# Performance work log

Hardware: AMD Instinct MI355X
Metric: run time of the kernel (lower is better)

Reference implementation:

```python
import jax, jax.numpy as jnp
import numpy as np

N_NODES = 50000
N_EDGES = 400000
D_NODE = 256
D_EDGE = 64
LN_EPS = 1e-6  # flax LayerNorm default


def _layer_norm(x, scale, bias):
    mu = jnp.mean(x, axis=-1, keepdims=True)
    var = jnp.mean(jnp.square(x - mu), axis=-1, keepdims=True)
    return (x - mu) * jax.lax.rsqrt(var + LN_EPS) * scale + bias


def _glorot(key, shape):
    fan_in, fan_out = shape
    std = jnp.sqrt(2.0 / (fan_in + fan_out))
    return std * jax.random.normal(key, shape, dtype=jnp.float32)


def setup_inputs() -> dict:
    key = jax.random.key(0)
    ks = jax.random.split(key, 10)
    inp = {
        "nodes": jax.random.normal(ks[0], (N_NODES, D_NODE), dtype=jnp.float32),
        "edges": jax.random.normal(ks[1], (N_EDGES, D_EDGE), dtype=jnp.float32),
        "senders": jax.random.randint(ks[2], (N_EDGES,), 0, N_NODES, dtype=jnp.int32),
        "receivers": jax.random.randint(ks[3], (N_EDGES,), 0, N_NODES, dtype=jnp.int32),
        # message projection (no bias)
        "W_message": _glorot(ks[4], (D_NODE + D_EDGE, D_NODE)),
        # NodeMLP (ReluMLP_skip) with n_features_list_nodes = [256, 256, 256]
        "mlp_W0": _glorot(ks[5], (D_NODE, D_NODE)), "mlp_b0": jnp.zeros((D_NODE,), jnp.float32),
        "mlp_W1": _glorot(ks[6], (D_NODE, D_NODE)), "mlp_b1": jnp.zeros((D_NODE,), jnp.float32),
        "mlp_W2": _glorot(ks[7], (D_NODE, D_NODE)), "mlp_b2": jnp.zeros((D_NODE,), jnp.float32),
        # LayerNorm params
        "ln_aggr_scale": jnp.ones((D_NODE,), jnp.float32), "ln_aggr_bias": jnp.zeros((D_NODE,), jnp.float32),
        "ln_out_scale": jnp.ones((D_NODE,), jnp.float32), "ln_out_bias": jnp.zeros((D_NODE,), jnp.float32),
    }
    return inp


def _relu_mlp_skip(x, Ws, bs):
    # Dense layers; ReLU on all but the last; residual add whenever widths match.
    n = len(Ws)
    for i, (W, b) in enumerate(zip(Ws, bs)):
        y = x @ W + b
        if i < n - 1:
            y = jax.nn.relu(y)
        x = x + y if y.shape[-1] == x.shape[-1] else y
    return x


def reference(nodes, edges, senders, receivers, W_message,
              mlp_W0, mlp_b0, mlp_W1, mlp_b1, mlp_W2, mlp_b2,
              ln_aggr_scale, ln_aggr_bias, ln_out_scale, ln_out_bias):
    total_nodes = nodes.shape[0]
    sender_features = nodes[senders]                      # [E, d] gather
    msg_in = jnp.concatenate([sender_features, edges], axis=-1)  # [E, d+d_e]
    messages = msg_in @ W_message                          # [E, d]
    agg = jax.ops.segment_sum(messages, receivers, num_segments=total_nodes)  # [N, d]
    h = _layer_norm(jax.nn.relu(agg) + nodes, ln_aggr_scale, ln_aggr_bias)
    nodes_out = _relu_mlp_skip(h, [mlp_W0, mlp_W1, mlp_W2], [mlp_b0, mlp_b1, mlp_b2])
    nodes_new = _layer_norm(nodes + nodes_out, ln_out_scale, ln_out_bias)
    return nodes_new
```

## Files before the change

### kernel.cpp

```cpp
#include <hip/hip_runtime.h>

#define NN 50000
#define NE 400000

typedef unsigned short u16;
typedef unsigned int   u32;
typedef __bf16 bf16x4 __attribute__((ext_vector_type(4)));
typedef __bf16 bf16x8 __attribute__((ext_vector_type(8)));
typedef float  f32x4  __attribute__((ext_vector_type(4)));

union ABFrag { bf16x8 v; bf16x4 h[2]; };
union BFrag  { uint4 u; bf16x8 v; };

__device__ __forceinline__ u16 f2bfu(float f) {
  u32 u = __builtin_bit_cast(u32, f);
  return (u16)((u + 0x7FFFu + ((u >> 16) & 1u)) >> 16);
}
__device__ __forceinline__ float bf2f(u16 u) {
  return __builtin_bit_cast(float, (u32)u << 16);
}

__device__ __forceinline__ void pack_one(const float* __restrict__ W,
                                         u16* __restrict__ P, int idx) {
  int k = idx >> 8, n = idx & 255;
  int t = k >> 5, kp = k & 31;
  int g = (kp & 15) >> 2;
  int j = (kp & 3) | ((kp >> 4) << 2);
  P[(((t << 8) + n) << 5) + (g << 3) + j] = f2bfu(W[idx]);
}

#define NB_CVT  12500
#define NB_PACK 1088
#define NB_HIST 1563

__global__ __launch_bounds__(256) void k_prep(
    const float* __restrict__ nodes, u16* __restrict__ nodes_bf,
    const float* __restrict__ Wm, const float* __restrict__ W0,
    const float* __restrict__ W1, const float* __restrict__ W2,
    u16* __restrict__ Pm, u16* __restrict__ P0,
    u16* __restrict__ P1, u16* __restrict__ P2,
    const int* __restrict__ recv, int* __restrict__ cnt)
{
  int b = blockIdx.x, t = threadIdx.x;
  if (b < NB_CVT) {
    int i = b * 256 + t;
    float4 f = ((const float4*)nodes)[i];
    ushort4 o;
    o.x = f2bfu(f.x); o.y = f2bfu(f.y); o.z = f2bfu(f.z); o.w = f2bfu(f.w);
    ((ushort4*)nodes_bf)[i] = o;
  } else if (b < NB_CVT + NB_PACK) {
    int idx = (b - NB_CVT) * 256 + t;
    const int S0 = 320 * 256, S1 = S0 + 65536, S2 = S1 + 65536;
    if (idx < S0)      pack_one(Wm, Pm, idx);
    else if (idx < S1) pack_one(W0, P0, idx - S0);
    else if (idx < S2) pack_one(W1, P1, idx - S1);
    else               pack_one(W2, P2, idx - S2);
  } else {
    int i = (b - NB_CVT - NB_PACK) * 256 + t;
    if (i < NE) atomicAdd(&cnt[recv[i]], 1);
  }
}

__global__ __launch_bounds__(256) void k_scan1(const int* __restrict__ cnt,
                                               int* __restrict__ loc,
                                               int* __restrict__ bsum) {
  __shared__ int sm[256];
  int t = threadIdx.x, i = blockIdx.x * 256 + t;
  int v = (i < NN) ? cnt[i] : 0;
  sm[t] = v;
  __syncthreads();
  #pragma unroll
  for (int d = 1; d < 256; d <<= 1) {
    int x = sm[t];
    int y = (t >= d) ? sm[t - d] : 0;
    __syncthreads();
    sm[t] = x + y;
    __syncthreads();
  }
  if (i < NN) loc[i] = sm[t] - v;
  if (t == 255) bsum[blockIdx.x] = sm[255];
}

__global__ __launch_bounds__(256) void k_scan2(int* __restrict__ bsum,
                                               int* __restrict__ bpre, int nb) {
  __shared__ int sm[256];
  int t = threadIdx.x;
  int v = (t < nb) ? bsum[t] : 0;
  sm[t] = v;
  __syncthreads();
  #pragma unroll
  for (int d = 1; d < 256; d <<= 1) {
    int x = sm[t];
    int y = (t >= d) ? sm[t - d] : 0;
    __syncthreads();
    sm[t] = x + y;
    __syncthreads();
  }
  if (t < nb) bpre[t] = sm[t] - v;
}

__global__ __launch_bounds__(256) void k_scan3(const int* __restrict__ loc,
                                               const int* __restrict__ bpre,
                                               int* __restrict__ offs,
                                               int* __restrict__ cursor) {
  int i = blockIdx.x * 256 + threadIdx.x;
  if (i < NN) {
    int o = loc[i] + bpre[blockIdx.x];
    offs[i] = o;
    cursor[i] = o;
  }
  if (i == NN - 1) offs[NN] = NE;
}

__global__ __launch_bounds__(256) void k_scatter(
    const int* __restrict__ snd, const int* __restrict__ recv,
    int* __restrict__ cursor, int* __restrict__ s_snd, int* __restrict__ s_eid) {
  int e = blockIdx.x * 256 + threadIdx.x;
  if (e < NE) {
    int p = atomicAdd(&cursor[recv[e]], 1);
    s_snd[p] = snd[e];
    s_eid[p] = e;
  }
}


#define AT_ADDR(r, c) (atb + ((((r) * 640) + ((c) * 2)) ^ (((r) & 7) << 4)))

#define WRBT(c, v) do { int _c = (c); \
  int _i = (((_c >> 10) << 13) + ((_c & 3) << 11) + (((_c & 1023) >> 2) << 3)) ^ ((_c & 3) << 4); \
  *(uint4*)&Bt[_i] = (v); } while (0)

#define MFMA_STEP(t) \
  _Pragma("unroll") \
  for (int kk = 0; kk < 2; ++kk) { \
    ABFrag a; \
    const int kc = (((t) * 2 + kk) << 5) + (g << 2); \
    const int m = wr16 + l16; \
    a.h[0] = *(const bf16x4*)AT_ADDR(m, kc); \
    a.h[1] = *(const bf16x4*)AT_ADDR(m, kc + 16); \
    _Pragma("unroll") \
    for (int q = 0; q < 4; ++q) { \
      BFrag b; \
      b.u = *(const uint4*)&Bt[((kk << 13) + (g << 11) + ((wcn + (q << 4) + l16) << 3)) ^ (g << 4)]; \
      acc[q] = __builtin_amdgcn_mfma_f32_16x16x32_bf16(a.v, b.v, acc[q], 0, 0, 0); \
    } \
  }

#define RUN_LAYER(wp, T) do { \
  const u16* pb = (wp) + ((size_t)tid << 3); \
  uint4 p0 = *(const uint4*)(pb); \
  uint4 p1 = *(const uint4*)(pb + 8192); \
  _Pragma("unroll 1") \
  for (int t = 0; t < (T); ++t) { \
    __syncthreads(); \
    WRBT(tid, p0); WRBT(tid + 1024, p1); \
    if (t + 1 < (T)) { \
      const u16* nb = pb + ((size_t)(t + 1) << 14); \
      p0 = *(const uint4*)nb; p1 = *(const uint4*)(nb + 8192); \
    } \
    __syncthreads(); \
    MFMA_STEP(t) \
  } \
} while (0)

#define LN_STATS() do { \
  _Pragma("unroll") \
  for (int r = 0; r < 4; ++r) { \
    float s  = acc[0][r] + acc[1][r] + acc[2][r] + acc[3][r]; \
    float s2 = acc[0][r]*acc[0][r] + acc[1][r]*acc[1][r] + acc[2][r]*acc[2][r] + acc[3][r]*acc[3][r]; \
    s  += __shfl_xor(s, 1);  s  += __shfl_xor(s, 2);  s  += __shfl_xor(s, 4);  s  += __shfl_xor(s, 8); \
    s2 += __shfl_xor(s2, 1); s2 += __shfl_xor(s2, 2); s2 += __shfl_xor(s2, 4); s2 += __shfl_xor(s2, 8); \
    if (l16 == 0) { int m = wr16 + g4 + r; red[m][wc2] = s; red[m][wc2 + 1] = s2; } \
  } \
  __syncthreads(); \
  if (tid < 64) { \
    float s  = red[tid][0] + red[tid][2] + red[tid][4] + red[tid][6]; \
    float s2 = red[tid][1] + red[tid][3] + red[tid][5] + red[tid][7]; \
    float mu  = s * (1.f / 256.f); \
    float var = s2 * (1.f / 256.f) - mu * mu; \
    murs[tid][0] = mu; murs[tid][1] = rsqrtf(var + 1e-6f); \
  } \
  __syncthreads(); \
} while (0)

__global__ __launch_bounds__(1024)
void k_fused(
    const u16* __restrict__ nodes_bf, const float* __restrict__ edges,
    const int* __restrict__ offs, const int* __restrict__ s_snd,
    const int* __restrict__ s_eid,
    const float* __restrict__ nodes,
    const u16* __restrict__ wm, const u16* __restrict__ w0,
    const u16* __restrict__ w1, const u16* __restrict__ w2,
    const float* __restrict__ b0, const float* __restrict__ b1,
    const float* __restrict__ b2,
    const float* __restrict__ lnAs, const float* __restrict__ lnAb,
    const float* __restrict__ lnOs, const float* __restrict__ lnOb,
    float* __restrict__ out)
{
  __shared__ u16 At[64 * 320];
  __shared__ u16 Bt[16384];
  __shared__ float red[64][8];
  __shared__ float murs[64][2];

  const int tid = threadIdx.x;
  const int lane = tid & 63;
  const int w16 = tid >> 6;
  const int wr16 = (w16 >> 2) << 4;
  const int wcn = (w16 & 3) << 6;
  const int wc2 = (w16 & 3) << 1;
  const int l16 = lane & 15, g = lane >> 4, g4 = g << 2;
  const int r0 = blockIdx.x * 64;

  char* const atb = (char*)At;

  {
    const int m0 = w16 << 2;
    #pragma unroll 1
    for (int i = 0; i < 4; ++i) {
      const int m = m0 + i;
      const int node = r0 + m;
      float a0 = 0.f, a1 = 0.f, a2 = 0.f, a3 = 0.f, a4 = 0.f;
      if (node < NN) {
        int beg = offs[node], end = offs[node + 1];
        int j = beg;
        for (; j + 1 < end; j += 2) {
          int sA = s_snd[j],     eA = s_eid[j];
          int sB = s_snd[j + 1], eB = s_eid[j + 1];
          ushort4 nA = *(const ushort4*)(nodes_bf + (size_t)sA * 256 + (lane << 2));
          ushort4 nB = *(const ushort4*)(nodes_bf + (size_t)sB * 256 + (lane << 2));
          float evA = edges[(size_t)eA * 64 + lane];
          float evB = edges[(size_t)eB * 64 + lane];
          a0 += bf2f(nA.x) + bf2f(nB.x); a1 += bf2f(nA.y) + bf2f(nB.y);
          a2 += bf2f(nA.z) + bf2f(nB.z); a3 += bf2f(nA.w) + bf2f(nB.w);
          a4 += evA + evB;
        }
        if (j < end) {
          int sA = s_snd[j], eA = s_eid[j];
          ushort4 nA = *(const ushort4*)(nodes_bf + (size_t)sA * 256 + (lane << 2));
          a0 += bf2f(nA.x); a1 += bf2f(nA.y); a2 += bf2f(nA.z); a3 += bf2f(nA.w);
          a4 += edges[(size_t)eA * 64 + lane];
        }
      }
      ushort4 o;
      o.x = f2bfu(a0); o.y = f2bfu(a1); o.z = f2bfu(a2); o.w = f2bfu(a3);
      *(ushort4*)AT_ADDR(m, lane << 2) = o;
      *(u16*)AT_ADDR(m, 256 + lane) = f2bfu(a4);
    }
  }

  f32x4 acc[4];
  const f32x4 z = {0.f, 0.f, 0.f, 0.f};
  #pragma unroll
  for (int q = 0; q < 4; ++q) acc[q] = z;

  RUN_LAYER(wm, 5);

  #pragma unroll
  for (int q = 0; q < 4; ++q) {
    int n = wcn + (q << 4) + l16;
    #pragma unroll
    for (int r = 0; r < 4; ++r) {
      int row = r0 + wr16 + g4 + r;
      float nv = (row < NN) ? nodes[(size_t)row * 256 + n] : 0.f;
      acc[q][r] = fmaxf(acc[q][r], 0.f) + nv;
    }
  }
  LN_STATS();
  #pragma unroll
  for (int q = 0; q < 4; ++q) {
    int n = wcn + (q << 4) + l16;
    float scl = lnAs[n], bia = lnAb[n];
    #pragma unroll
    for (int r = 0; r < 4; ++r) {
      int m = wr16 + g4 + r;
      float h = (acc[q][r] - murs[m][0]) * murs[m][1] * scl + bia;
      *(u16*)AT_ADDR(m, n) = f2bfu(h);
      acc[q][r] = 0.f;
    }
  }

  #pragma unroll 1
  for (int l = 0; l < 3; ++l) {
    const u16* wp = (l == 0) ? w0 : (l == 1) ? w1 : w2;
    RUN_LAYER(wp, 4);
    __syncthreads();

    if (l < 2) {
      const float* bp = (l == 0) ? b0 : b1;
      #pragma unroll
      for (int q = 0; q < 4; ++q) {
        int n = wcn + (q << 4) + l16;
        float bn = bp[n];
        #pragma unroll
        for (int r = 0; r < 4; ++r) {
          int m = wr16 + g4 + r;
          u16* p = (u16*)AT_ADDR(m, n);
          float xn = bf2f(*p) + fmaxf(acc[q][r] + bn, 0.f);
          *p = f2bfu(xn);
          acc[q][r] = 0.f;
        }
      }
    } else {
      #pragma unroll
      for (int q = 0; q < 4; ++q) {
        int n = wcn + (q << 4) + l16;
        float bn = b2[n];
        #pragma unroll
        for (int r = 0; r < 4; ++r) {
          int m = wr16 + g4 + r;
          int row = r0 + m;
          float nv = (row < NN) ? nodes[(size_t)row * 256 + n] : 0.f;
          acc[q][r] = nv + bf2f(*(const u16*)AT_ADDR(m, n)) + acc[q][r] + bn;
        }
      }
    }
  }

  LN_STATS();
  #pragma unroll
  for (int q = 0; q < 4; ++q) {
    int n = wcn + (q << 4) + l16;
    float scl = lnOs[n], bia = lnOb[n];
    #pragma unroll
    for (int r = 0; r < 4; ++r) {
      int m = wr16 + g4 + r;
      int row = r0 + m;
      if (row < NN)
        out[(size_t)row * 256 + n] =
            (acc[q][r] - murs[m][0]) * murs[m][1] * scl + bia;
    }
  }
}

extern "C" void kernel_launch(void* const* d_in, const int* in_sizes, int n_in,
                              void* d_out, int out_size, void* d_ws, size_t ws_size,
                              hipStream_t stream)
{
  const float* nodes = (const float*)d_in[0];
  const float* edges = (const float*)d_in[1];
  const int* senders = (const int*)d_in[2];
  const int* receivers = (const int*)d_in[3];
  const float* Wmsg = (const float*)d_in[4];
  const float* W0 = (const float*)d_in[5];
  const float* b0 = (const float*)d_in[6];
  const float* W1 = (const float*)d_in[7];
  const float* b1 = (const float*)d_in[8];
  const float* W2 = (const float*)d_in[9];
  const float* b2 = (const float*)d_in[10];
  const float* lnAs = (const float*)d_in[11];
  const float* lnAb = (const float*)d_in[12];
  const float* lnOs = (const float*)d_in[13];
  const float* lnOb = (const float*)d_in[14];
  float* out = (float*)d_out;
  (void)in_sizes; (void)n_in; (void)out_size; (void)ws_size;

  char* w = (char*)d_ws;
  size_t off = 0;
  auto take = [&](size_t b) { void* p = w + off; off += (b + 511) & ~(size_t)511; return p; };

  u16*   nodes_bf = (u16*)take((size_t)NN * 256 * 2);
  u16*   wmsg_p   = (u16*)take(320 * 256 * 2);
  u16*   w0_p     = (u16*)take(256 * 256 * 2);
  u16*   w1_p     = (u16*)take(256 * 256 * 2);
  u16*   w2_p     = (u16*)take(256 * 256 * 2);
  int*   cnt      = (int*)take((size_t)NN * 4);
  int*   loc      = (int*)take((size_t)NN * 4);
  int*   offs     = (int*)take((size_t)(NN + 1) * 4);
  int*   cursor   = (int*)take((size_t)NN * 4);
  int*   s_snd    = (int*)take((size_t)NE * 4);
  int*   s_eid    = (int*)take((size_t)NE * 4);
  int*   bsum     = (int*)take(256 * 4);
  int*   bpre     = (int*)take(256 * 4);

  const int NB = (NN + 255) / 256;

  hipMemsetAsync(cnt, 0, (size_t)NN * 4, stream);
  k_prep<<<NB_CVT + NB_PACK + NB_HIST, 256, 0, stream>>>(
      nodes, nodes_bf, Wmsg, W0, W1, W2, wmsg_p, w0_p, w1_p, w2_p,
      receivers, cnt);

  k_scan1<<<NB, 256, 0, stream>>>(cnt, loc, bsum);
  k_scan2<<<1, 256, 0, stream>>>(bsum, bpre, NB);
  k_scan3<<<NB, 256, 0, stream>>>(loc, bpre, offs, cursor);
  k_scatter<<<(NE + 255) / 256, 256, 0, stream>>>(senders, receivers, cursor, s_snd, s_eid);

  const int MB = (NN + 63) / 64;
  k_fused<<<MB, 1024, 0, stream>>>(nodes_bf, edges, offs, s_snd, s_eid,
                                   nodes, wmsg_p, w0_p, w1_p, w2_p,
                                   b0, b1, b2, lnAs, lnAb, lnOs, lnOb, out);
}
```

Before: 235.2 us.

## Split gather-aggregation into separate prefetching kernel before fused MLP kernel

Moves the per-node gather/sum of sender features and edge features out of the fused GEMM kernel into a new k_aggr kernel. It processes 4 consecutive nodes per wavefront with a software-pipelined, 4-deep prefetch of edge loads and writes a bf16 [N,320] buffer. The fused kernel then just loads that buffer into LDS, so its 1024-thread blocks no longer stall on irregular gathers. The weight prefetch in the layer loop is moved after the second barrier. This costs an extra ~32MB write+read round trip through global memory and one more kernel launch.

```diff
diff --git a/kernel.cpp b/kernel.cpp
--- a/kernel.cpp
+++ b/kernel.cpp
@@ -123,6 +123,60 @@
   }
 }
 
+__global__ __launch_bounds__(256) void k_aggr(
+    const u16* __restrict__ nodes_bf, const float* __restrict__ edges,
+    const int* __restrict__ offs, const int* __restrict__ s_snd,
+    const int* __restrict__ s_eid, u16* __restrict__ X)
+{
+  const int wid = blockIdx.x * 4 + (threadIdx.x >> 6);
+  const int lane = threadIdx.x & 63;
+  const int n0 = wid * 4;
+  const int o0 = offs[n0], b1 = offs[n0 + 1], b2 = offs[n0 + 2],
+            b3 = offs[n0 + 3], o4 = offs[n0 + 4];
+
+  float a0 = 0.f, a1 = 0.f, a2 = 0.f, a3 = 0.f, a4 = 0.f;
+  int cur = 0;
+
+#define AGLD(J, NV, EV) do { int _j = (J); if (_j < o4) { \
+    int _s = s_snd[_j], _e = s_eid[_j]; \
+    NV = *(const ushort4*)(nodes_bf + (size_t)_s * 256 + (lane << 2)); \
+    EV = edges[(size_t)_e * 64 + lane]; } } while (0)
+
+#define AGFLUSH(NODE) do { \
+    ushort4 _o; _o.x = f2bfu(a0); _o.y = f2bfu(a1); _o.z = f2bfu(a2); _o.w = f2bfu(a3); \
+    u16* _xr = X + (size_t)(NODE) * 320; \
+    *(ushort4*)(_xr + (lane << 2)) = _o; \
+    _xr[256 + lane] = f2bfu(a4); \
+    a0 = 0.f; a1 = 0.f; a2 = 0.f; a3 = 0.f; a4 = 0.f; } while (0)
+
+#define AGCONS(J, NV, EV) do { int _j = (J); if (_j < o4) { \
+    if (cur == 0 && _j == b1) { AGFLUSH(n0);     cur = 1; } \
+    if (cur == 1 && _j == b2) { AGFLUSH(n0 + 1); cur = 2; } \
+    if (cur == 2 && _j == b3) { AGFLUSH(n0 + 2); cur = 3; } \
+    a0 += bf2f(NV.x); a1 += bf2f(NV.y); a2 += bf2f(NV.z); a3 += bf2f(NV.w); \
+    a4 += EV; } } while (0)
+
+  ushort4 v0 = {0,0,0,0}, v1 = {0,0,0,0}, v2 = {0,0,0,0}, v3 = {0,0,0,0};
+  float e0 = 0.f, e1 = 0.f, e2 = 0.f, e3 = 0.f;
+  AGLD(o0 + 0, v0, e0); AGLD(o0 + 1, v1, e1);
+  AGLD(o0 + 2, v2, e2); AGLD(o0 + 3, v3, e3);
+
+  for (int jb = o0; jb < o4; jb += 4) {
+    ushort4 w0 = {0,0,0,0}, w1 = {0,0,0,0}, w2 = {0,0,0,0}, w3 = {0,0,0,0};
+    float f0 = 0.f, f1 = 0.f, f2 = 0.f, f3 = 0.f;
+    AGLD(jb + 4, w0, f0); AGLD(jb + 5, w1, f1);
+    AGLD(jb + 6, w2, f2); AGLD(jb + 7, w3, f3);
+    AGCONS(jb + 0, v0, e0); AGCONS(jb + 1, v1, e1);
+    AGCONS(jb + 2, v2, e2); AGCONS(jb + 3, v3, e3);
+    v0 = w0; v1 = w1; v2 = w2; v3 = w3;
+    e0 = f0; e1 = f1; e2 = f2; e3 = f3;
+  }
+  for (int k = cur; k < 4; ++k) AGFLUSH(n0 + k);
+#undef AGLD
+#undef AGFLUSH
+#undef AGCONS
+}
+
 
 #define AT_ADDR(r, c) (atb + ((((r) * 640) + ((c) * 2)) ^ (((r) & 7) << 4)))
 
@@ -154,11 +208,11 @@
   for (int t = 0; t < (T); ++t) { \
     __syncthreads(); \
     WRBT(tid, p0); WRBT(tid + 1024, p1); \
-    if (t + 1 < (T)) { \
+    __syncthreads(); \
+    if (t + 1 < (T)) {                      \
       const u16* nb = pb + ((size_t)(t + 1) << 14); \
       p0 = *(const uint4*)nb; p1 = *(const uint4*)(nb + 8192); \
     } \
-    __syncthreads(); \
     MFMA_STEP(t) \
   } \
 } while (0)
@@ -185,10 +239,7 @@
 
 __global__ __launch_bounds__(1024)
 void k_fused(
-    const u16* __restrict__ nodes_bf, const float* __restrict__ edges,
-    const int* __restrict__ offs, const int* __restrict__ s_snd,
-    const int* __restrict__ s_eid,
-    const float* __restrict__ nodes,
+    const u16* __restrict__ X, const float* __restrict__ nodes,
     const u16* __restrict__ wm, const u16* __restrict__ w0,
     const u16* __restrict__ w1, const u16* __restrict__ w2,
     const float* __restrict__ b0, const float* __restrict__ b1,
@@ -213,38 +264,15 @@
 
   char* const atb = (char*)At;
 
-  {
-    const int m0 = w16 << 2;
-    #pragma unroll 1
-    for (int i = 0; i < 4; ++i) {
-      const int m = m0 + i;
-      const int node = r0 + m;
-      float a0 = 0.f, a1 = 0.f, a2 = 0.f, a3 = 0.f, a4 = 0.f;
-      if (node < NN) {
-        int beg = offs[node], end = offs[node + 1];
-        int j = beg;
-        for (; j + 1 < end; j += 2) {
-          int sA = s_snd[j],     eA = s_eid[j];
-          int sB = s_snd[j + 1], eB = s_eid[j + 1];
-          ushort4 nA = *(const ushort4*)(nodes_bf + (size_t)sA * 256 + (lane << 2));
-          ushort4 nB = *(const ushort4*)(nodes_bf + (size_t)sB * 256 + (lane << 2));
-          float evA = edges[(size_t)eA * 64 + lane];
-          float evB = edges[(size_t)eB * 64 + lane];
-          a0 += bf2f(nA.x) + bf2f(nB.x); a1 += bf2f(nA.y) + bf2f(nB.y);
-          a2 += bf2f(nA.z) + bf2f(nB.z); a3 += bf2f(nA.w) + bf2f(nB.w);
-          a4 += evA + evB;
-        }
-        if (j < end) {
-          int sA = s_snd[j], eA = s_eid[j];
-          ushort4 nA = *(const ushort4*)(nodes_bf + (size_t)sA * 256 + (lane << 2));
-          a0 += bf2f(nA.x); a1 += bf2f(nA.y); a2 += bf2f(nA.z); a3 += bf2f(nA.w);
-          a4 += edges[(size_t)eA * 64 + lane];
-        }
-      }
-      ushort4 o;
-      o.x = f2bfu(a0); o.y = f2bfu(a1); o.z = f2bfu(a2); o.w = f2bfu(a3);
-      *(ushort4*)AT_ADDR(m, lane << 2) = o;
-      *(u16*)AT_ADDR(m, 256 + lane) = f2bfu(a4);
+  #pragma unroll
+  for (int it = 0; it < 3; ++it) {
+    int c = tid + it * 1024;
+    if (c < 2560) {
+      int r = c / 40, seg = c - r * 40;
+      int row = r0 + r;
+      uint4 v = {0u, 0u, 0u, 0u};
+      if (row < NN) v = *(const uint4*)(X + (size_t)row * 320 + seg * 8);
+      *(uint4*)(atb + ((r * 640 + seg * 16) ^ ((r & 7) << 4))) = v;
     }
   }
 
@@ -363,6 +391,7 @@
   u16*   w0_p     = (u16*)take(256 * 256 * 2);
   u16*   w1_p     = (u16*)take(256 * 256 * 2);
   u16*   w2_p     = (u16*)take(256 * 256 * 2);
+  u16*   X        = (u16*)take((size_t)NN * 320 * 2);
   int*   cnt      = (int*)take((size_t)NN * 4);
   int*   loc      = (int*)take((size_t)NN * 4);
   int*   offs     = (int*)take((size_t)(NN + 1) * 4);
@@ -384,8 +413,9 @@
   k_scan3<<<NB, 256, 0, stream>>>(loc, bpre, offs, cursor);
   k_scatter<<<(NE + 255) / 256, 256, 0, stream>>>(senders, receivers, cursor, s_snd, s_eid);
 
+  k_aggr<<<NN / 16, 256, 0, stream>>>(nodes_bf, edges, offs, s_snd, s_eid, X);
+
   const int MB = (NN + 63) / 64;
-  k_fused<<<MB, 1024, 0, stream>>>(nodes_bf, edges, offs, s_snd, s_eid,
-                                   nodes, wmsg_p, w0_p, w1_p, w2_p,
+  k_fused<<<MB, 1024, 0, stream>>>(X, nodes, wmsg_p, w0_p, w1_p, w2_p,
                                    b0, b1, b2, lnAs, lnAb, lnOs, lnOb, out);
 }
```

After: 248.4 us. 1.06x slower.
